# Kernel optimization log

Measured on AMD Instinct MI355X. Metric: run time of the kernel, lower is better.

## Reference

```python
import jax, jax.numpy as jnp
import numpy as np

TOP_K = 2
EPS = 1e-06


def setup_inputs() -> dict:
    key = jax.random.key(0)
    k1, k2 = jax.random.split(key)
    x = jax.random.normal(k1, (4, 8192, 1024), dtype=jnp.float32)
    # nn.Linear weight: [num_experts, d_model]
    W = jax.random.normal(k2, (64, 1024), dtype=jnp.float32) * (1.0 / np.sqrt(1024))
    return {"x": x, "W": W}


def reference(x, W):
    # router logits: (b, s, e)
    logits = jnp.einsum('bsd,ed->bse', x, W)
    # top-k selection (values sorted descending, like torch.topk)
    top_vals, top_idx = jax.lax.top_k(logits, TOP_K)
    top_gates = jax.nn.softmax(top_vals, axis=-1)
    # load-balance loss over full softmax probs
    probs = jax.nn.softmax(logits, axis=-1)
    avg_probs = probs.mean(axis=(0, 1))  # (e,)
    # torch.std defaults to unbiased (ddof=1)
    loss = (jnp.std(avg_probs, ddof=1) / (avg_probs.mean() + EPS)) ** 2
    return (top_idx, top_gates, loss)
```

## Files before the change

### kernel.cpp

```cpp
#include <hip/hip_runtime.h>
#include <math.h>
#include <stdint.h>


constexpr int DMODEL = 1024;
constexpr int NEXP   = 64;
constexpr int BM     = 64;
constexpr int BK     = 64;
constexpr int NTOK   = 32768;
constexpr int NTILE  = DMODEL / BK;

constexpr int XS   = 0;
constexpr int XSB  = 64 * 64 * 4;
constexpr int WS   = 32768;
constexpr int WSB  = 3 * 64 * 64 * 2;
constexpr int WCMP = 64 * 64 * 2;
constexpr int LSTR = 68 * 4;

constexpr size_t WSPLIT_OFF   = 256;
constexpr size_t WSPLIT_BYTES = (size_t)NTILE * WSB;

typedef __attribute__((ext_vector_type(8))) short short8;
typedef __attribute__((ext_vector_type(4))) float f32x4;

__device__ __forceinline__ void gload16(const void* g, void* l) {
    __builtin_amdgcn_global_load_lds(
        (const __attribute__((address_space(1))) unsigned int*)g,
        (__attribute__((address_space(3))) unsigned int*)l,
        16, 0, 0);
}

__device__ __forceinline__ void split3(float x, short& h, short& m, short& l) {
    uint32_t u  = __float_as_uint(x);
    uint32_t uh = u & 0xffff0000u;
    float    r  = x - __uint_as_float(uh);
    uint32_t ur = __float_as_uint(r);
    uint32_t um = ur & 0xffff0000u;
    float    r2 = r - __uint_as_float(um);
    h = (short)(uh >> 16);
    m = (short)(um >> 16);
    l = (short)(__float_as_uint(r2) >> 16);
}

__global__ void wsplit_kernel(const float* __restrict__ W, char* __restrict__ dst)
{
    const int g = blockIdx.x * 256 + threadIdx.x;
    const int e = g >> 7;
    const int c = g & 127;
    const int tile = c >> 3;
    const int q    = c & 7;
    const float* src = W + (size_t)e * DMODEL + c * 8;
    const float4 a = *reinterpret_cast<const float4*>(src);
    const float4 b = *reinterpret_cast<const float4*>(src + 4);
    short8 sH, sM, sL;
    const float v[8] = {a.x, a.y, a.z, a.w, b.x, b.y, b.z, b.w};
#pragma unroll
    for (int j = 0; j < 8; ++j) {
        short h, m, l; split3(v[j], h, m, l);
        sH[j] = h; sM[j] = m; sL[j] = l;
    }
    char* base = dst + (size_t)tile * WSB + e * 128 + ((q ^ (e & 7)) << 4);
    *reinterpret_cast<short8*>(base)            = sH;
    *reinterpret_cast<short8*>(base + WCMP)     = sM;
    *reinterpret_cast<short8*>(base + 2 * WCMP) = sL;
}

__global__ __launch_bounds__(512, 2) void router_kernel(
    const float* __restrict__ x, const char* __restrict__ wsAll,
    float* __restrict__ out, float* __restrict__ expert_sums)
{
    __shared__ __align__(16) char smem[81920];

    const int tid  = threadIdx.x;
    const int lane = tid & 63;
    const int w    = tid >> 6;
    const int mt   = w & 3;
    const int kh   = w >> 2;
    const int tok0 = blockIdx.x * BM;

    f32x4 acc[4];
#pragma unroll
    for (int nt = 0; nt < 4; ++nt) acc[nt] = (f32x4){0.f, 0.f, 0.f, 0.f};

    auto stageX = [&](int buf, int tile) {
#pragma unroll
        for (int i = 0; i < 2; ++i) {
            const int r0 = w * 8 + i * 4;
            const int r  = r0 + (lane >> 4);
            const int c  = lane & 15;
            const float* src = x + (size_t)(tok0 + r) * DMODEL + tile * BK
                                 + ((c ^ (r & 15)) << 2);
            gload16(src, smem + XS + buf * XSB + r0 * 256 + (lane << 4));
        }
    };
    auto stageW = [&](int buf, int tile) {
        const char* src = wsAll + (size_t)tile * WSB + w * 1024 + (lane << 4);
        char* dst = smem + WS + buf * WSB + w * 1024 + (lane << 4);
#pragma unroll
        for (int j = 0; j < 3; ++j)
            gload16(src + j * WCMP, dst + j * WCMP);
    };

    stageX(0, 0);
    stageW(0, 0);

    int buf = 0;
    for (int tile = 0; tile < NTILE; ++tile) {
        if (tile + 1 < NTILE) {
            stageX(buf ^ 1, tile + 1);
            stageW(buf ^ 1, tile + 1);
            asm volatile("s_waitcnt vmcnt(5)" ::: "memory");
        } else {
            asm volatile("s_waitcnt vmcnt(0)" ::: "memory");
        }
        __builtin_amdgcn_sched_barrier(0);
        __builtin_amdgcn_s_barrier();

        {
            const int ks = kh;
            const int rl = mt * 16 + (lane & 15);
            const int c0 = ks * 8 + (lane >> 4) * 2;
            const char* xrow = smem + XS + buf * XSB + rl * 256;
            const float4 xa = *reinterpret_cast<const float4*>(
                xrow + ((c0 ^ (lane & 15)) << 4));
            const float4 xb = *reinterpret_cast<const float4*>(
                xrow + (((c0 + 1) ^ (lane & 15)) << 4));
            short8 aH, aM, aL;
            {
                float v[8] = {xa.x, xa.y, xa.z, xa.w, xb.x, xb.y, xb.z, xb.w};
#pragma unroll
                for (int j = 0; j < 8; ++j) {
                    short h, m, l; split3(v[j], h, m, l);
                    aH[j] = h; aM[j] = m; aL[j] = l;
                }
            }
#pragma unroll
            for (int nt = 0; nt < 4; ++nt) {
                const int ef = nt * 16 + (lane & 15);
                const int q  = ks * 4 + (lane >> 4);
                const char* wrow = smem + WS + buf * WSB + ef * 128
                                 + ((q ^ (ef & 7)) << 4);
                const short8 bH = *reinterpret_cast<const short8*>(wrow);
                const short8 bM = *reinterpret_cast<const short8*>(wrow + WCMP);
                const short8 bL = *reinterpret_cast<const short8*>(wrow + 2 * WCMP);
                acc[nt] = __builtin_amdgcn_mfma_f32_16x16x32_bf16(aH, bH, acc[nt], 0, 0, 0);
                acc[nt] = __builtin_amdgcn_mfma_f32_16x16x32_bf16(aH, bM, acc[nt], 0, 0, 0);
                acc[nt] = __builtin_amdgcn_mfma_f32_16x16x32_bf16(aM, bH, acc[nt], 0, 0, 0);
                acc[nt] = __builtin_amdgcn_mfma_f32_16x16x32_bf16(aH, bL, acc[nt], 0, 0, 0);
                acc[nt] = __builtin_amdgcn_mfma_f32_16x16x32_bf16(aM, bM, acc[nt], 0, 0, 0);
                acc[nt] = __builtin_amdgcn_mfma_f32_16x16x32_bf16(aL, bH, acc[nt], 0, 0, 0);
            }
        }
        __builtin_amdgcn_s_barrier();
        buf ^= 1;
    }

    if (kh == 0) {
#pragma unroll
        for (int nt = 0; nt < 4; ++nt)
#pragma unroll
            for (int r = 0; r < 4; ++r) {
                const int t = mt * 16 + (lane >> 4) * 4 + r;
                const int e = nt * 16 + (lane & 15);
                *reinterpret_cast<float*>(smem + t * LSTR + e * 4) = acc[nt][r];
            }
    }
    __syncthreads();
    if (kh == 1) {
#pragma unroll
        for (int nt = 0; nt < 4; ++nt)
#pragma unroll
            for (int r = 0; r < 4; ++r) {
                const int t = mt * 16 + (lane >> 4) * 4 + r;
                const int e = nt * 16 + (lane & 15);
                float* p = reinterpret_cast<float*>(smem + t * LSTR + e * 4);
                *p += acc[nt][r];
            }
    }
    __syncthreads();

    float* maxArr = reinterpret_cast<float*>(smem + 18432);
    float* invArr = reinterpret_cast<float*>(smem + 18688);
    float* psum   = reinterpret_cast<float*>(smem + 18944);

    if (tid < BM) {
        const char* lrow = smem + tid * LSTR;
        float4 L[16];
#pragma unroll
        for (int i = 0; i < 16; ++i)
            L[i] = *reinterpret_cast<const float4*>(lrow + i * 16);

        float mx = -INFINITY;
#pragma unroll
        for (int i = 0; i < 16; ++i)
            mx = fmaxf(mx, fmaxf(fmaxf(L[i].x, L[i].y), fmaxf(L[i].z, L[i].w)));

        float v0 = -INFINITY, v1 = -INFINITY;
        int   i0 = NEXP, i1 = NEXP;
        float s = 0.f;
#pragma unroll
        for (int i = 0; i < 16; ++i) {
            const float vv[4] = {L[i].x, L[i].y, L[i].z, L[i].w};
#pragma unroll
            for (int c = 0; c < 4; ++c) {
                const float v = vv[c];
                const int  gi = i * 4 + c;
                s += __expf(v - mx);
                if (v > v0) { v1 = v0; i1 = i0; v0 = v; i0 = gi; }
                else if (v > v1) { v1 = v; i1 = gi; }
            }
        }
        maxArr[tid] = mx;
        invArr[tid] = 1.0f / s;

        const float q = __expf(v1 - v0);
        const float d = 1.0f + q;
        const size_t tok = (size_t)tok0 + tid;
        reinterpret_cast<float2*>(out)[tok]            = make_float2((float)i0, (float)i1);
        reinterpret_cast<float2*>(out + 2 * NTOK)[tok] = make_float2(1.0f / d, q / d);
    }
    __syncthreads();

    {
        const int e = tid & 63, grp = tid >> 6;
        float s = 0.f;
#pragma unroll
        for (int i = 0; i < 8; ++i) {
            const int t = grp * 8 + i;
            const float lg = *reinterpret_cast<const float*>(smem + t * LSTR + e * 4);
            s += __expf(lg - maxArr[t]) * invArr[t];
        }
        psum[grp * 64 + e] = s;
    }
    __syncthreads();
    if (tid < 64) {
        float s = 0.f;
#pragma unroll
        for (int g = 0; g < 8; ++g) s += psum[g * 64 + tid];
        atomicAdd(&expert_sums[tid], s);
    }
}

__global__ __launch_bounds__(512, 2) void router_fallback(
    const float* __restrict__ x, const float* __restrict__ W,
    float* __restrict__ out, float* __restrict__ expert_sums)
{
    __shared__ __align__(16) char smem[81920];

    const int tid  = threadIdx.x;
    const int lane = tid & 63;
    const int w    = tid >> 6;
    const int mt   = w & 3;
    const int kh   = w >> 2;
    const int tok0 = blockIdx.x * BM;

    f32x4 acc[4];
#pragma unroll
    for (int nt = 0; nt < 4; ++nt) acc[nt] = (f32x4){0.f, 0.f, 0.f, 0.f};

    auto stageX = [&](int buf, int tile) {
#pragma unroll
        for (int i = 0; i < 2; ++i) {
            const int r0 = w * 8 + i * 4;
            const int r  = r0 + (lane >> 4);
            const int c  = lane & 15;
            const float* src = x + (size_t)(tok0 + r) * DMODEL + tile * BK
                                 + ((c ^ (r & 15)) << 2);
            gload16(src, smem + XS + buf * XSB + r0 * 256 + (lane << 4));
        }
    };

    const int we  = tid >> 3;
    const int wc  = tid & 7;
    const int wph = wc ^ (we & 7);
    const float* wgp = W + (size_t)we * DMODEL + wc * 8;

    auto convW = [&](int buf, float4 a, float4 b) {
        short8 sH, sM, sL;
        float v[8] = {a.x, a.y, a.z, a.w, b.x, b.y, b.z, b.w};
#pragma unroll
        for (int j = 0; j < 8; ++j) {
            short h, m, l; split3(v[j], h, m, l);
            sH[j] = h; sM[j] = m; sL[j] = l;
        }
        char* d = smem + WS + buf * WSB + we * 128 + wph * 16;
        *reinterpret_cast<short8*>(d)             = sH;
        *reinterpret_cast<short8*>(d + WCMP)      = sM;
        *reinterpret_cast<short8*>(d + 2 * WCMP)  = sL;
    };

    stageX(0, 0);
    {
        float4 a = *reinterpret_cast<const float4*>(wgp);
        float4 b = *reinterpret_cast<const float4*>(wgp + 4);
        convW(0, a, b);
    }
    __syncthreads();

    int buf = 0;
    for (int tile = 0; tile < NTILE; ++tile) {
        float4 wa, wb;
        if (tile + 1 < NTILE) {
            stageX(buf ^ 1, tile + 1);
            wa = *reinterpret_cast<const float4*>(wgp + (tile + 1) * BK);
            wb = *reinterpret_cast<const float4*>(wgp + (tile + 1) * BK + 4);
        }
        {
            const int ks = kh;
            const int rl = mt * 16 + (lane & 15);
            const int c0 = ks * 8 + (lane >> 4) * 2;
            const char* xrow = smem + XS + buf * XSB + rl * 256;
            const float4 xa = *reinterpret_cast<const float4*>(
                xrow + ((c0 ^ (lane & 15)) << 4));
            const float4 xb = *reinterpret_cast<const float4*>(
                xrow + (((c0 + 1) ^ (lane & 15)) << 4));
            short8 aH, aM, aL;
            {
                float v[8] = {xa.x, xa.y, xa.z, xa.w, xb.x, xb.y, xb.z, xb.w};
#pragma unroll
                for (int j = 0; j < 8; ++j) {
                    short h, m, l; split3(v[j], h, m, l);
                    aH[j] = h; aM[j] = m; aL[j] = l;
                }
            }
#pragma unroll
            for (int nt = 0; nt < 4; ++nt) {
                const int ef = nt * 16 + (lane & 15);
                const int q  = ks * 4 + (lane >> 4);
                const char* wrow = smem + WS + buf * WSB + ef * 128
                                 + ((q ^ (ef & 7)) << 4);
                const short8 bH = *reinterpret_cast<const short8*>(wrow);
                const short8 bM = *reinterpret_cast<const short8*>(wrow + WCMP);
                const short8 bL = *reinterpret_cast<const short8*>(wrow + 2 * WCMP);
                acc[nt] = __builtin_amdgcn_mfma_f32_16x16x32_bf16(aH, bH, acc[nt], 0, 0, 0);
                acc[nt] = __builtin_amdgcn_mfma_f32_16x16x32_bf16(aH, bM, acc[nt], 0, 0, 0);
                acc[nt] = __builtin_amdgcn_mfma_f32_16x16x32_bf16(aM, bH, acc[nt], 0, 0, 0);
                acc[nt] = __builtin_amdgcn_mfma_f32_16x16x32_bf16(aH, bL, acc[nt], 0, 0, 0);
                acc[nt] = __builtin_amdgcn_mfma_f32_16x16x32_bf16(aM, bM, acc[nt], 0, 0, 0);
                acc[nt] = __builtin_amdgcn_mfma_f32_16x16x32_bf16(aL, bH, acc[nt], 0, 0, 0);
            }
        }
        if (tile + 1 < NTILE) convW(buf ^ 1, wa, wb);
        __syncthreads();
        buf ^= 1;
    }

    if (kh == 0) {
#pragma unroll
        for (int nt = 0; nt < 4; ++nt)
#pragma unroll
            for (int r = 0; r < 4; ++r) {
                const int t = mt * 16 + (lane >> 4) * 4 + r;
                const int e = nt * 16 + (lane & 15);
                *reinterpret_cast<float*>(smem + t * LSTR + e * 4) = acc[nt][r];
            }
    }
    __syncthreads();
    if (kh == 1) {
#pragma unroll
        for (int nt = 0; nt < 4; ++nt)
#pragma unroll
            for (int r = 0; r < 4; ++r) {
                const int t = mt * 16 + (lane >> 4) * 4 + r;
                const int e = nt * 16 + (lane & 15);
                float* p = reinterpret_cast<float*>(smem + t * LSTR + e * 4);
                *p += acc[nt][r];
            }
    }
    __syncthreads();

    float* maxArr = reinterpret_cast<float*>(smem + 18432);
    float* invArr = reinterpret_cast<float*>(smem + 18688);
    float* psum   = reinterpret_cast<float*>(smem + 18944);

    if (tid < BM) {
        const char* lrow = smem + tid * LSTR;
        float4 L[16];
#pragma unroll
        for (int i = 0; i < 16; ++i)
            L[i] = *reinterpret_cast<const float4*>(lrow + i * 16);
        float mx = -INFINITY;
#pragma unroll
        for (int i = 0; i < 16; ++i)
            mx = fmaxf(mx, fmaxf(fmaxf(L[i].x, L[i].y), fmaxf(L[i].z, L[i].w)));
        float v0 = -INFINITY, v1 = -INFINITY;
        int   i0 = NEXP, i1 = NEXP;
        float s = 0.f;
#pragma unroll
        for (int i = 0; i < 16; ++i) {
            const float vv[4] = {L[i].x, L[i].y, L[i].z, L[i].w};
#pragma unroll
            for (int c = 0; c < 4; ++c) {
                const float v = vv[c];
                const int  gi = i * 4 + c;
                s += __expf(v - mx);
                if (v > v0) { v1 = v0; i1 = i0; v0 = v; i0 = gi; }
                else if (v > v1) { v1 = v; i1 = gi; }
            }
        }
        maxArr[tid] = mx;
        invArr[tid] = 1.0f / s;
        const float q = __expf(v1 - v0);
        const float d = 1.0f + q;
        const size_t tok = (size_t)tok0 + tid;
        reinterpret_cast<float2*>(out)[tok]            = make_float2((float)i0, (float)i1);
        reinterpret_cast<float2*>(out + 2 * NTOK)[tok] = make_float2(1.0f / d, q / d);
    }
    __syncthreads();
    {
        const int e = tid & 63, grp = tid >> 6;
        float s = 0.f;
#pragma unroll
        for (int i = 0; i < 8; ++i) {
            const int t = grp * 8 + i;
            const float lg = *reinterpret_cast<const float*>(smem + t * LSTR + e * 4);
            s += __expf(lg - maxArr[t]) * invArr[t];
        }
        psum[grp * 64 + e] = s;
    }
    __syncthreads();
    if (tid < 64) {
        float s = 0.f;
#pragma unroll
        for (int g = 0; g < 8; ++g) s += psum[g * 64 + tid];
        atomicAdd(&expert_sums[tid], s);
    }
}

__global__ void loss_kernel(const float* __restrict__ sums, float* __restrict__ out)
{
    const int lane = threadIdx.x;
    float pv = sums[lane] * (1.0f / (float)NTOK);
    float m = pv;
#pragma unroll
    for (int off = 32; off; off >>= 1) m += __shfl_xor(m, off, 64);
    m *= (1.0f / (float)NEXP);
    float d = pv - m;
    float v = d * d;
#pragma unroll
    for (int off = 32; off; off >>= 1) v += __shfl_xor(v, off, 64);
    v *= (1.0f / (float)(NEXP - 1));
    if (lane == 0) {
        float stdv = sqrtf(v);
        float r = stdv / (m + 1e-6f);
        out[4 * NTOK] = r * r;
    }
}

extern "C" void kernel_launch(void* const* d_in, const int* in_sizes, int n_in,
                              void* d_out, int out_size, void* d_ws, size_t ws_size,
                              hipStream_t stream)
{
    const float* x = (const float*)d_in[0];
    const float* W = (const float*)d_in[1];
    float* out  = (float*)d_out;
    float* sums = (float*)d_ws;

    hipMemsetAsync(d_ws, 0, 256, stream);

    if (ws_size >= WSPLIT_OFF + WSPLIT_BYTES) {
        char* wsAll = (char*)d_ws + WSPLIT_OFF;
        hipLaunchKernelGGL(wsplit_kernel, dim3(32), dim3(256), 0, stream, W, wsAll);
        hipLaunchKernelGGL(router_kernel, dim3(NTOK / BM), dim3(512), 0, stream,
                           x, wsAll, out, sums);
    } else {
        hipLaunchKernelGGL(router_fallback, dim3(NTOK / BM), dim3(512), 0, stream,
                           x, W, out, sums);
    }
    hipLaunchKernelGGL(loss_kernel, dim3(1), dim3(64), 0, stream, sums, out);
}
```

Before: 51.57 us.

## Load pre-split W fragments straight into registers with 4-wave blocks

The pre-split bf16 W is laid out in per-lane MFMA fragment order, so each wave loads its B operands directly from global memory into registers instead of staging them through LDS. Blocks drop from 8 to 4 waves. Each wave now covers all four row tiles for half the experts on one K-half, which reuses each split x fragment across two expert tiles and cuts LDS use to about 34 KB. The cost is more registers per thread, a deeper vmcnt pipeline, and a full unroll of the tile loop.

After: 55.37 us. +7.4%, slower.

```diff
diff --git a/kernel.cpp b/kernel.cpp
--- a/kernel.cpp
+++ b/kernel.cpp
@@ -10,15 +10,9 @@
 constexpr int NTOK   = 32768;
 constexpr int NTILE  = DMODEL / BK;
 
-constexpr int XS   = 0;
-constexpr int XSB  = 64 * 64 * 4;
-constexpr int WS   = 32768;
-constexpr int WSB  = 3 * 64 * 64 * 2;
-constexpr int WCMP = 64 * 64 * 2;
 constexpr int LSTR = 68 * 4;
-
 constexpr size_t WSPLIT_OFF   = 256;
-constexpr size_t WSPLIT_BYTES = (size_t)NTILE * WSB;
+constexpr size_t WSPLIT_BYTES = 384 * 1024;
 
 typedef __attribute__((ext_vector_type(8))) short short8;
 typedef __attribute__((ext_vector_type(4))) float f32x4;
@@ -47,8 +41,12 @@
     const int g = blockIdx.x * 256 + threadIdx.x;
     const int e = g >> 7;
     const int c = g & 127;
-    const int tile = c >> 3;
-    const int q    = c & 7;
+    const int T   = c >> 3;
+    const int q   = c & 7;
+    const int ks  = q >> 2;
+    const int qhi = q & 3;
+    const int lane = (qhi << 4) | (e & 15);
+    const int nt   = e >> 4;
     const float* src = W + (size_t)e * DMODEL + c * 8;
     const float4 a = *reinterpret_cast<const float4*>(src);
     const float4 b = *reinterpret_cast<const float4*>(src + 4);
@@ -59,14 +57,202 @@
         short h, m, l; split3(v[j], h, m, l);
         sH[j] = h; sM[j] = m; sL[j] = l;
     }
-    char* base = dst + (size_t)tile * WSB + e * 128 + ((q ^ (e & 7)) << 4);
-    *reinterpret_cast<short8*>(base)            = sH;
-    *reinterpret_cast<short8*>(base + WCMP)     = sM;
-    *reinterpret_cast<short8*>(base + 2 * WCMP) = sL;
-}
-
-__global__ __launch_bounds__(512, 2) void router_kernel(
+    char* base = dst + ((size_t)((T * 2 + ks) * 4 + nt) * 3) * 1024
+                     + (size_t)lane * 16;
+    *reinterpret_cast<short8*>(base)        = sH;
+    *reinterpret_cast<short8*>(base + 1024) = sM;
+    *reinterpret_cast<short8*>(base + 2048) = sL;
+}
+
+__global__ __launch_bounds__(256, 2) void router_kernel(
     const float* __restrict__ x, const char* __restrict__ wsAll,
+    float* __restrict__ out, float* __restrict__ expert_sums)
+{
+    __shared__ __align__(16) char smem[34304];
+
+    const int tid  = threadIdx.x;
+    const int lane = tid & 63;
+    const int w    = tid >> 6;
+    const int ks   = w & 1;
+    const int nh   = w >> 1;
+    const int tok0 = blockIdx.x * BM;
+
+    f32x4 acc[4][2];
+#pragma unroll
+    for (int mt = 0; mt < 4; ++mt)
+#pragma unroll
+        for (int j = 0; j < 2; ++j) acc[mt][j] = (f32x4){0.f, 0.f, 0.f, 0.f};
+
+    auto stageX = [&](int buf, int tile) {
+#pragma unroll
+        for (int i = 0; i < 4; ++i) {
+            const int flat = i * 256 + tid;
+            const int r = flat >> 4;
+            const int c = flat & 15;
+            const float* src = x + (size_t)(tok0 + r) * DMODEL + tile * BK
+                                 + ((c ^ (r & 15)) << 2);
+            gload16(src, smem + buf * 16384 + i * 4096 + tid * 16);
+        }
+    };
+    auto loadW = [&](short8* bank, int tile) {
+#pragma unroll
+        for (int j = 0; j < 2; ++j)
+#pragma unroll
+            for (int cp = 0; cp < 3; ++cp) {
+                const int fi = ((tile * 2 + ks) * 4 + (nh * 2 + j)) * 3 + cp;
+                bank[j * 3 + cp] = *reinterpret_cast<const short8*>(
+                    wsAll + (size_t)fi * 1024 + (size_t)lane * 16);
+            }
+    };
+
+    short8 wb[2][6];
+    stageX(0, 0);
+    loadW(wb[0], 0);
+
+#pragma unroll
+    for (int t = 0; t < NTILE; ++t) {
+        if (t + 1 < NTILE) {
+            stageX((t + 1) & 1, t + 1);
+            loadW(wb[(t + 1) & 1], t + 1);
+        }
+        if (t < NTILE - 1) asm volatile("s_waitcnt vmcnt(10)" ::: "memory");
+        else               asm volatile("s_waitcnt vmcnt(0)"  ::: "memory");
+        __builtin_amdgcn_sched_barrier(0);
+        __builtin_amdgcn_s_barrier();
+        __builtin_amdgcn_sched_barrier(0);
+
+#pragma unroll
+        for (int mt = 0; mt < 4; ++mt) {
+            const int rl = mt * 16 + (lane & 15);
+            const int c0 = ks * 8 + (lane >> 4) * 2;
+            const char* xrow = smem + (t & 1) * 16384 + rl * 256;
+            const float4 xa = *reinterpret_cast<const float4*>(
+                xrow + ((c0 ^ (rl & 15)) << 4));
+            const float4 xb = *reinterpret_cast<const float4*>(
+                xrow + (((c0 + 1) ^ (rl & 15)) << 4));
+            short8 aH, aM, aL;
+            {
+                const float v[8] = {xa.x, xa.y, xa.z, xa.w, xb.x, xb.y, xb.z, xb.w};
+#pragma unroll
+                for (int jj = 0; jj < 8; ++jj) {
+                    short h, m, l; split3(v[jj], h, m, l);
+                    aH[jj] = h; aM[jj] = m; aL[jj] = l;
+                }
+            }
+#pragma unroll
+            for (int j = 0; j < 2; ++j) {
+                const short8 bH = wb[t & 1][j * 3 + 0];
+                const short8 bM = wb[t & 1][j * 3 + 1];
+                const short8 bL = wb[t & 1][j * 3 + 2];
+                acc[mt][j] = __builtin_amdgcn_mfma_f32_16x16x32_bf16(aH, bH, acc[mt][j], 0, 0, 0);
+                acc[mt][j] = __builtin_amdgcn_mfma_f32_16x16x32_bf16(aH, bM, acc[mt][j], 0, 0, 0);
+                acc[mt][j] = __builtin_amdgcn_mfma_f32_16x16x32_bf16(aM, bH, acc[mt][j], 0, 0, 0);
+                acc[mt][j] = __builtin_amdgcn_mfma_f32_16x16x32_bf16(aH, bL, acc[mt][j], 0, 0, 0);
+                acc[mt][j] = __builtin_amdgcn_mfma_f32_16x16x32_bf16(aM, bM, acc[mt][j], 0, 0, 0);
+                acc[mt][j] = __builtin_amdgcn_mfma_f32_16x16x32_bf16(aL, bH, acc[mt][j], 0, 0, 0);
+            }
+        }
+        __builtin_amdgcn_sched_barrier(0);
+        __builtin_amdgcn_s_barrier();
+        __builtin_amdgcn_sched_barrier(0);
+    }
+
+    if (ks == 0) {
+#pragma unroll
+        for (int mt = 0; mt < 4; ++mt)
+#pragma unroll
+            for (int j = 0; j < 2; ++j)
+#pragma unroll
+                for (int r = 0; r < 4; ++r) {
+                    const int tk = mt * 16 + (lane >> 4) * 4 + r;
+                    const int e  = (nh * 2 + j) * 16 + (lane & 15);
+                    *reinterpret_cast<float*>(smem + tk * LSTR + e * 4) = acc[mt][j][r];
+                }
+    }
+    __syncthreads();
+    if (ks == 1) {
+#pragma unroll
+        for (int mt = 0; mt < 4; ++mt)
+#pragma unroll
+            for (int j = 0; j < 2; ++j)
+#pragma unroll
+                for (int r = 0; r < 4; ++r) {
+                    const int tk = mt * 16 + (lane >> 4) * 4 + r;
+                    const int e  = (nh * 2 + j) * 16 + (lane & 15);
+                    float* p = reinterpret_cast<float*>(smem + tk * LSTR + e * 4);
+                    *p += acc[mt][j][r];
+                }
+    }
+    __syncthreads();
+
+    float* maxArr = reinterpret_cast<float*>(smem + 32768);
+    float* invArr = reinterpret_cast<float*>(smem + 33024);
+    float* psum   = reinterpret_cast<float*>(smem + 33280);
+
+    if (tid < BM) {
+        const char* lrow = smem + tid * LSTR;
+        float4 L[16];
+#pragma unroll
+        for (int i = 0; i < 16; ++i)
+            L[i] = *reinterpret_cast<const float4*>(lrow + i * 16);
+
+        float mx = -INFINITY;
+#pragma unroll
+        for (int i = 0; i < 16; ++i)
+            mx = fmaxf(mx, fmaxf(fmaxf(L[i].x, L[i].y), fmaxf(L[i].z, L[i].w)));
+
+        float v0 = -INFINITY, v1 = -INFINITY;
+        int   i0 = NEXP, i1 = NEXP;
+        float s = 0.f;
+#pragma unroll
+        for (int i = 0; i < 16; ++i) {
+            const float vv[4] = {L[i].x, L[i].y, L[i].z, L[i].w};
+#pragma unroll
+            for (int c = 0; c < 4; ++c) {
+                const float v = vv[c];
+                const int  gi = i * 4 + c;
+                s += __expf(v - mx);
+                if (v > v0) { v1 = v0; i1 = i0; v0 = v; i0 = gi; }
+                else if (v > v1) { v1 = v; i1 = gi; }
+            }
+        }
+        maxArr[tid] = mx;
+        invArr[tid] = 1.0f / s;
+
+        const float q = __expf(v1 - v0);
+        const float d = 1.0f + q;
+        const size_t tok = (size_t)tok0 + tid;
+        reinterpret_cast<float2*>(out)[tok]            = make_float2((float)i0, (float)i1);
+        reinterpret_cast<float2*>(out + 2 * NTOK)[tok] = make_float2(1.0f / d, q / d);
+    }
+    __syncthreads();
+
+    {
+        const int e = tid & 63, grp = tid >> 6;
+        float s = 0.f;
+#pragma unroll
+        for (int i = 0; i < 16; ++i) {
+            const int tk = grp * 16 + i;
+            const float lg = *reinterpret_cast<const float*>(smem + tk * LSTR + e * 4);
+            s += __expf(lg - maxArr[tk]) * invArr[tk];
+        }
+        psum[grp * 64 + e] = s;
+    }
+    __syncthreads();
+    if (tid < 64) {
+        const float s = (psum[tid] + psum[64 + tid]) + (psum[128 + tid] + psum[192 + tid]);
+        atomicAdd(&expert_sums[tid], s);
+    }
+}
+
+constexpr int FXS   = 0;
+constexpr int FXSB  = 64 * 64 * 4;
+constexpr int FWS   = 32768;
+constexpr int FWSB  = 3 * 64 * 64 * 2;
+constexpr int FWCMP = 64 * 64 * 2;
+
+__global__ __launch_bounds__(512, 2) void router_fallback(
+    const float* __restrict__ x, const float* __restrict__ W,
     float* __restrict__ out, float* __restrict__ expert_sums)
 {
     __shared__ __align__(16) char smem[81920];
@@ -90,183 +276,7 @@
             const int c  = lane & 15;
             const float* src = x + (size_t)(tok0 + r) * DMODEL + tile * BK
                                  + ((c ^ (r & 15)) << 2);
-            gload16(src, smem + XS + buf * XSB + r0 * 256 + (lane << 4));
-        }
-    };
-    auto stageW = [&](int buf, int tile) {
-        const char* src = wsAll + (size_t)tile * WSB + w * 1024 + (lane << 4);
-        char* dst = smem + WS + buf * WSB + w * 1024 + (lane << 4);
-#pragma unroll
-        for (int j = 0; j < 3; ++j)
-            gload16(src + j * WCMP, dst + j * WCMP);
-    };
-
-    stageX(0, 0);
-    stageW(0, 0);
-
-    int buf = 0;
-    for (int tile = 0; tile < NTILE; ++tile) {
-        if (tile + 1 < NTILE) {
-            stageX(buf ^ 1, tile + 1);
-            stageW(buf ^ 1, tile + 1);
-            asm volatile("s_waitcnt vmcnt(5)" ::: "memory");
-        } else {
-            asm volatile("s_waitcnt vmcnt(0)" ::: "memory");
-        }
-        __builtin_amdgcn_sched_barrier(0);
-        __builtin_amdgcn_s_barrier();
-
-        {
-            const int ks = kh;
-            const int rl = mt * 16 + (lane & 15);
-            const int c0 = ks * 8 + (lane >> 4) * 2;
-            const char* xrow = smem + XS + buf * XSB + rl * 256;
-            const float4 xa = *reinterpret_cast<const float4*>(
-                xrow + ((c0 ^ (lane & 15)) << 4));
-            const float4 xb = *reinterpret_cast<const float4*>(
-                xrow + (((c0 + 1) ^ (lane & 15)) << 4));
-            short8 aH, aM, aL;
-            {
-                float v[8] = {xa.x, xa.y, xa.z, xa.w, xb.x, xb.y, xb.z, xb.w};
-#pragma unroll
-                for (int j = 0; j < 8; ++j) {
-                    short h, m, l; split3(v[j], h, m, l);
-                    aH[j] = h; aM[j] = m; aL[j] = l;
-                }
-            }
-#pragma unroll
-            for (int nt = 0; nt < 4; ++nt) {
-                const int ef = nt * 16 + (lane & 15);
-                const int q  = ks * 4 + (lane >> 4);
-                const char* wrow = smem + WS + buf * WSB + ef * 128
-                                 + ((q ^ (ef & 7)) << 4);
-                const short8 bH = *reinterpret_cast<const short8*>(wrow);
-                const short8 bM = *reinterpret_cast<const short8*>(wrow + WCMP);
-                const short8 bL = *reinterpret_cast<const short8*>(wrow + 2 * WCMP);
-                acc[nt] = __builtin_amdgcn_mfma_f32_16x16x32_bf16(aH, bH, acc[nt], 0, 0, 0);
-                acc[nt] = __builtin_amdgcn_mfma_f32_16x16x32_bf16(aH, bM, acc[nt], 0, 0, 0);
-                acc[nt] = __builtin_amdgcn_mfma_f32_16x16x32_bf16(aM, bH, acc[nt], 0, 0, 0);
-                acc[nt] = __builtin_amdgcn_mfma_f32_16x16x32_bf16(aH, bL, acc[nt], 0, 0, 0);
-                acc[nt] = __builtin_amdgcn_mfma_f32_16x16x32_bf16(aM, bM, acc[nt], 0, 0, 0);
-                acc[nt] = __builtin_amdgcn_mfma_f32_16x16x32_bf16(aL, bH, acc[nt], 0, 0, 0);
-            }
-        }
-        __builtin_amdgcn_s_barrier();
-        buf ^= 1;
-    }
-
-    if (kh == 0) {
-#pragma unroll
-        for (int nt = 0; nt < 4; ++nt)
-#pragma unroll
-            for (int r = 0; r < 4; ++r) {
-                const int t = mt * 16 + (lane >> 4) * 4 + r;
-                const int e = nt * 16 + (lane & 15);
-                *reinterpret_cast<float*>(smem + t * LSTR + e * 4) = acc[nt][r];
-            }
-    }
-    __syncthreads();
-    if (kh == 1) {
-#pragma unroll
-        for (int nt = 0; nt < 4; ++nt)
-#pragma unroll
-            for (int r = 0; r < 4; ++r) {
-                const int t = mt * 16 + (lane >> 4) * 4 + r;
-                const int e = nt * 16 + (lane & 15);
-                float* p = reinterpret_cast<float*>(smem + t * LSTR + e * 4);
-                *p += acc[nt][r];
-            }
-    }
-    __syncthreads();
-
-    float* maxArr = reinterpret_cast<float*>(smem + 18432);
-    float* invArr = reinterpret_cast<float*>(smem + 18688);
-    float* psum   = reinterpret_cast<float*>(smem + 18944);
-
-    if (tid < BM) {
-        const char* lrow = smem + tid * LSTR;
-        float4 L[16];
-#pragma unroll
-        for (int i = 0; i < 16; ++i)
-            L[i] = *reinterpret_cast<const float4*>(lrow + i * 16);
-
-        float mx = -INFINITY;
-#pragma unroll
-        for (int i = 0; i < 16; ++i)
-            mx = fmaxf(mx, fmaxf(fmaxf(L[i].x, L[i].y), fmaxf(L[i].z, L[i].w)));
-
-        float v0 = -INFINITY, v1 = -INFINITY;
-        int   i0 = NEXP, i1 = NEXP;
-        float s = 0.f;
-#pragma unroll
-        for (int i = 0; i < 16; ++i) {
-            const float vv[4] = {L[i].x, L[i].y, L[i].z, L[i].w};
-#pragma unroll
-            for (int c = 0; c < 4; ++c) {
-                const float v = vv[c];
-                const int  gi = i * 4 + c;
-                s += __expf(v - mx);
-                if (v > v0) { v1 = v0; i1 = i0; v0 = v; i0 = gi; }
-                else if (v > v1) { v1 = v; i1 = gi; }
-            }
-        }
-        maxArr[tid] = mx;
-        invArr[tid] = 1.0f / s;
-
-        const float q = __expf(v1 - v0);
-        const float d = 1.0f + q;
-        const size_t tok = (size_t)tok0 + tid;
-        reinterpret_cast<float2*>(out)[tok]            = make_float2((float)i0, (float)i1);
-        reinterpret_cast<float2*>(out + 2 * NTOK)[tok] = make_float2(1.0f / d, q / d);
-    }
-    __syncthreads();
-
-    {
-        const int e = tid & 63, grp = tid >> 6;
-        float s = 0.f;
-#pragma unroll
-        for (int i = 0; i < 8; ++i) {
-            const int t = grp * 8 + i;
-            const float lg = *reinterpret_cast<const float*>(smem + t * LSTR + e * 4);
-            s += __expf(lg - maxArr[t]) * invArr[t];
-        }
-        psum[grp * 64 + e] = s;
-    }
-    __syncthreads();
-    if (tid < 64) {
-        float s = 0.f;
-#pragma unroll
-        for (int g = 0; g < 8; ++g) s += psum[g * 64 + tid];
-        atomicAdd(&expert_sums[tid], s);
-    }
-}
-
-__global__ __launch_bounds__(512, 2) void router_fallback(
-    const float* __restrict__ x, const float* __restrict__ W,
-    float* __restrict__ out, float* __restrict__ expert_sums)
-{
-    __shared__ __align__(16) char smem[81920];
-
-    const int tid  = threadIdx.x;
-    const int lane = tid & 63;
-    const int w    = tid >> 6;
-    const int mt   = w & 3;
-    const int kh   = w >> 2;
-    const int tok0 = blockIdx.x * BM;
-
-    f32x4 acc[4];
-#pragma unroll
-    for (int nt = 0; nt < 4; ++nt) acc[nt] = (f32x4){0.f, 0.f, 0.f, 0.f};
-
-    auto stageX = [&](int buf, int tile) {
-#pragma unroll
-        for (int i = 0; i < 2; ++i) {
-            const int r0 = w * 8 + i * 4;
-            const int r  = r0 + (lane >> 4);
-            const int c  = lane & 15;
-            const float* src = x + (size_t)(tok0 + r) * DMODEL + tile * BK
-                                 + ((c ^ (r & 15)) << 2);
-            gload16(src, smem + XS + buf * XSB + r0 * 256 + (lane << 4));
+            gload16(src, smem + FXS + buf * FXSB + r0 * 256 + (lane << 4));
         }
     };
 
@@ -283,10 +293,10 @@
             short h, m, l; split3(v[j], h, m, l);
             sH[j] = h; sM[j] = m; sL[j] = l;
         }
-        char* d = smem + WS + buf * WSB + we * 128 + wph * 16;
-        *reinterpret_cast<short8*>(d)             = sH;
-        *reinterpret_cast<short8*>(d + WCMP)      = sM;
-        *reinterpret_cast<short8*>(d + 2 * WCMP)  = sL;
+        char* d = smem + FWS + buf * FWSB + we * 128 + wph * 16;
+        *reinterpret_cast<short8*>(d)            = sH;
+        *reinterpret_cast<short8*>(d + FWCMP)    = sM;
+        *reinterpret_cast<short8*>(d + 2 * FWCMP) = sL;
     };
 
     stageX(0, 0);
@@ -306,14 +316,14 @@
             wb = *reinterpret_cast<const float4*>(wgp + (tile + 1) * BK + 4);
         }
         {
-            const int ks = kh;
+            const int ksl = kh;
             const int rl = mt * 16 + (lane & 15);
-            const int c0 = ks * 8 + (lane >> 4) * 2;
-            const char* xrow = smem + XS + buf * XSB + rl * 256;
+            const int c0 = ksl * 8 + (lane >> 4) * 2;
+            const char* xrow = smem + FXS + buf * FXSB + rl * 256;
             const float4 xa = *reinterpret_cast<const float4*>(
-                xrow + ((c0 ^ (lane & 15)) << 4));
+                xrow + ((c0 ^ (rl & 15)) << 4));
             const float4 xb = *reinterpret_cast<const float4*>(
-                xrow + (((c0 + 1) ^ (lane & 15)) << 4));
+                xrow + (((c0 + 1) ^ (rl & 15)) << 4));
             short8 aH, aM, aL;
             {
                 float v[8] = {xa.x, xa.y, xa.z, xa.w, xb.x, xb.y, xb.z, xb.w};
@@ -326,12 +336,12 @@
 #pragma unroll
             for (int nt = 0; nt < 4; ++nt) {
                 const int ef = nt * 16 + (lane & 15);
-                const int q  = ks * 4 + (lane >> 4);
-                const char* wrow = smem + WS + buf * WSB + ef * 128
+                const int q  = ksl * 4 + (lane >> 4);
+                const char* wrow = smem + FWS + buf * FWSB + ef * 128
                                  + ((q ^ (ef & 7)) << 4);
                 const short8 bH = *reinterpret_cast<const short8*>(wrow);
-                const short8 bM = *reinterpret_cast<const short8*>(wrow + WCMP);
-                const short8 bL = *reinterpret_cast<const short8*>(wrow + 2 * WCMP);
+                const short8 bM = *reinterpret_cast<const short8*>(wrow + FWCMP);
+                const short8 bL = *reinterpret_cast<const short8*>(wrow + 2 * FWCMP);
                 acc[nt] = __builtin_amdgcn_mfma_f32_16x16x32_bf16(aH, bH, acc[nt], 0, 0, 0);
                 acc[nt] = __builtin_amdgcn_mfma_f32_16x16x32_bf16(aH, bM, acc[nt], 0, 0, 0);
                 acc[nt] = __builtin_amdgcn_mfma_f32_16x16x32_bf16(aM, bH, acc[nt], 0, 0, 0);
@@ -461,7 +471,7 @@
     if (ws_size >= WSPLIT_OFF + WSPLIT_BYTES) {
         char* wsAll = (char*)d_ws + WSPLIT_OFF;
         hipLaunchKernelGGL(wsplit_kernel, dim3(32), dim3(256), 0, stream, W, wsAll);
-        hipLaunchKernelGGL(router_kernel, dim3(NTOK / BM), dim3(512), 0, stream,
+        hipLaunchKernelGGL(router_kernel, dim3(NTOK / BM), dim3(256), 0, stream,
                            x, wsAll, out, sums);
     } else {
         hipLaunchKernelGGL(router_fallback, dim3(NTOK / BM), dim3(512), 0, stream,
```
